# Kernel tuning notes

Hardware: AMD Instinct MI355X
Metric: run time of the kernel (lower is better)

The kernel has to match this reference:

```python
import jax, jax.numpy as jnp
import numpy as np

HIDDEN = 51
INPUT = 1
OUTPUT = 1
BATCH = 4096
SEQ = 999


def setup_inputs() -> dict:
    key = jax.random.key(0)
    ks = jax.random.split(key, 7)
    s = 1.0 / np.sqrt(HIDDEN)  # PyTorch default LSTM/Linear init scale
    u = lambda k, shape: jax.random.uniform(k, shape, jnp.float32, -s, s)
    return {
        "input": jax.random.normal(ks[0], (BATCH, SEQ, INPUT), jnp.float32),
        "W_ih": u(ks[1], (4 * HIDDEN, INPUT)),
        "W_hh": u(ks[2], (4 * HIDDEN, HIDDEN)),
        "b_ih": u(ks[3], (4 * HIDDEN,)),
        "b_hh": u(ks[4], (4 * HIDDEN,)),
        "W_fc": u(ks[5], (OUTPUT, HIDDEN)),
        "b_fc": u(ks[6], (OUTPUT,)),
        "future": 0,
    }


def reference(input, W_ih, W_hh, b_ih, b_hh, W_fc, b_fc, future):
    # Single-layer LSTM (PyTorch gate order i, f, g, o) scanned over time,
    # followed by a per-timestep Linear -> (batch, seq+future, output).
    def step(carry, x_t):
        h, c = carry
        gates = x_t @ W_ih.T + b_ih + h @ W_hh.T + b_hh  # (B, 4H)
        i, f, g, o = jnp.split(gates, 4, axis=-1)
        c = jax.nn.sigmoid(f) * c + jax.nn.sigmoid(i) * jnp.tanh(g)
        h = jax.nn.sigmoid(o) * jnp.tanh(c)
        return (h, c), h

    B = input.shape[0]
    h0 = jnp.zeros((B, HIDDEN), input.dtype)
    c0 = jnp.zeros((B, HIDDEN), input.dtype)
    xs = jnp.swapaxes(input, 0, 1)  # (T, B, I)
    (h, c), hs = jax.lax.scan(step, (h0, c0), xs)
    ys = hs @ W_fc.T + b_fc  # (T, B, O)

    # static Python int, so a trace-time loop is fine).
    y = ys[-1]
    extra = []
    for _ in range(future):
        (h, c), hn = step((h, c), y)
        y = hn @ W_fc.T + b_fc
        extra.append(y)
    if extra:
        ys = jnp.concatenate([ys, jnp.stack(extra, 0)], axis=0)
    return jnp.swapaxes(ys, 0, 1)  # (B, T+future, O)
```

## Files before the change

### kernel.cpp

```cpp
#include <hip/hip_runtime.h>
#include <hip/hip_bf16.h>

#define HID   51
#define MR    208
#define SEQT  999
#define CH    111
#define NCH   9
#define EPB   16
#define XST   17
#define NTH   448
#define BSTR  72

typedef __attribute__((ext_vector_type(8))) short  short8;
typedef __attribute__((ext_vector_type(4))) float  floatx4;
typedef __attribute__((ext_vector_type(2))) float  floatx2;

__global__ void prep_kernel(const float* __restrict__ W_hh,
                            const float* __restrict__ W_ih,
                            const float* __restrict__ W_fc,
                            __hip_bfloat16* __restrict__ A_ext)
{
    const float K1 = 1.442695040889f;
    int idx = blockIdx.x * blockDim.x + threadIdx.x;
    if (idx >= MR * 64) return;
    int r = idx >> 6, k = idx & 63;
    int T = r >> 4, r16 = r & 15, g4r = r16 >> 2, gate = r16 & 3;
    float v = 0.f;
    if (T < 12) {
        int u = ((T >> 1) << 3) + 2 * g4r + (T & 1);
        float s = (gate == 2) ? (-2.f * K1) : (-K1);
        if (k < HID)      v = s * W_hh[(gate * HID + u) * HID + k];
        else if (k == 51) v = s * W_ih[gate * HID + u];
    } else {
        if (g4r < 3) {
            int u = 48 + g4r;
            float s = (gate == 2) ? (-2.f * K1) : (-K1);
            if (k < HID)      v = s * W_hh[(gate * HID + u) * HID + k];
            else if (k == 51) v = s * W_ih[gate * HID + u];
        } else if (gate == 0) {
            if (k < HID) v = W_fc[k];
        }
    }
    A_ext[idx] = __float2bfloat16(v);
}

__launch_bounds__(NTH)
__global__ void lstm_mfma_kernel(const float* __restrict__ x,
                                 const float* __restrict__ b_ih,
                                 const float* __restrict__ b_hh,
                                 const float* __restrict__ b_fc,
                                 const __hip_bfloat16* __restrict__ A_ext,
                                 float* __restrict__ out)
{
    __shared__ __hip_bfloat16 bcol[2][16 * BSTR];
    __shared__ float x_lds[(CH + 1) * XST];
    __shared__ float y_lds[CH * XST];

    const int tid  = threadIdx.x;
    const int w    = tid >> 6;
    const int lane = tid & 63;
    const int e    = lane & 15;
    const int g4   = lane >> 4;
    const int e0   = blockIdx.x * EPB;
    const bool w6  = (w == 6);
    const int  uB6   = 48 + g4;
    const bool yln   = w6 && (g4 == 3);
    const bool xsv   = w6 && (g4 == 0);
    const int  wrow6 = (uB6 < HID) ? uB6 : 63;

    const float K1  = 1.442695040889f;
    const float K2N = -2.885390081777f;
    const floatx4 z4 = {0.f, 0.f, 0.f, 0.f};

    short8  A0a = {0,0,0,0,0,0,0,0}, A1a = {0,0,0,0,0,0,0,0};
    short8  A0b = {0,0,0,0,0,0,0,0}, A1b = {0,0,0,0,0,0,0,0};
    floatx4 bqa = {0.f, 0.f, 0.f, 0.f}, bqb = {0.f, 0.f, 0.f, 0.f};
    floatx2 cs2 = {0.f, 0.f};
    float   cs6 = 0.f;
    int ua = 0;

    if (!w6) {
        int Ta = 2 * w, Tb = 2 * w + 1;
        ua = 8 * w + 2 * g4;
        int ma = Ta * 16 + e, mb = Tb * 16 + e;
        A0a = *(const short8*)&A_ext[ma * 64 + g4 * 8];
        A1a = *(const short8*)&A_ext[ma * 64 + 32 + g4 * 8];
        A0b = *(const short8*)&A_ext[mb * 64 + g4 * 8];
        A1b = *(const short8*)&A_ext[mb * 64 + 32 + g4 * 8];
#pragma unroll
        for (int gg = 0; gg < 4; ++gg) {
            float s = (gg == 2) ? (-2.f * K1) : (-K1);
            bqa[gg] = s * (b_ih[gg * HID + ua]     + b_hh[gg * HID + ua]);
            bqb[gg] = s * (b_ih[gg * HID + ua + 1] + b_hh[gg * HID + ua + 1]);
        }
    } else {
        int m = 12 * 16 + e;
        A0a = *(const short8*)&A_ext[m * 64 + g4 * 8];
        A1a = *(const short8*)&A_ext[m * 64 + 32 + g4 * 8];
        if (uB6 < HID) {
#pragma unroll
            for (int gg = 0; gg < 4; ++gg) {
                float s = (gg == 2) ? (-2.f * K1) : (-K1);
                bqa[gg] = s * (b_ih[gg * HID + uB6] + b_hh[gg * HID + uB6]);
            }
        }
    }

    for (int i = tid; i < 16 * BSTR; i += NTH) {
        bcol[0][i] = __float2bfloat16(0.f);
        bcol[1][i] = __float2bfloat16(0.f);
    }
    __syncthreads();
    if (tid < EPB)
        bcol[0][tid * BSTR + 51] = __float2bfloat16(x[(size_t)(e0 + tid) * SEQT]);
    for (int i2 = tid; i2 < (CH + 1) * EPB; i2 += NTH) {
        int ee = i2 / (CH + 1), tt = i2 % (CH + 1);
        x_lds[tt * XST + ee] = x[(size_t)(e0 + ee) * SEQT + tt];
    }
    const float bfc = b_fc[0];

    __syncthreads();

    for (int tc = 0; tc < NCH; ++tc) {
        const int t0 = tc * CH;

        float xpre[4];
        {
            const int t0n = t0 + CH;
#pragma unroll
            for (int q = 0; q < 4; ++q) {
                int i2 = tid + q * NTH;
                int ee = i2 / (CH + 1), tt = i2 - ee * (CH + 1);
                int t = t0n + tt;
                xpre[q] = (t < SEQT) ? x[(size_t)(e0 + ee) * SEQT + t] : 0.f;
            }
        }

        for (int tt = 0; tt < CH; ++tt) {
            const int t  = t0 + tt;
            const int rp = t & 1, wp = rp ^ 1;

            short8 B0 = *(const short8*)&bcol[rp][e * BSTR + g4 * 8];
            short8 B1 = *(const short8*)&bcol[rp][e * BSTR + 32 + g4 * 8];

            if (!w6) {
                floatx4 aa = __builtin_amdgcn_mfma_f32_16x16x32_bf16(A0a, B0, bqa, 0, 0, 0);
                floatx4 a2 = __builtin_amdgcn_mfma_f32_16x16x32_bf16(A1a, B1, z4,  0, 0, 0);
                floatx4 ab = __builtin_amdgcn_mfma_f32_16x16x32_bf16(A0b, B0, bqb, 0, 0, 0);
                floatx4 b2 = __builtin_amdgcn_mfma_f32_16x16x32_bf16(A1b, B1, z4,  0, 0, 0);

                floatx4 sa = aa + a2;
                floatx4 sb = ab + b2;

                float EiA = __builtin_amdgcn_exp2f(sa[0]);
                float EiB = __builtin_amdgcn_exp2f(sb[0]);
                float EfA = __builtin_amdgcn_exp2f(sa[1]);
                float EfB = __builtin_amdgcn_exp2f(sb[1]);
                float EgA = __builtin_amdgcn_exp2f(sa[2]);
                float EgB = __builtin_amdgcn_exp2f(sb[2]);
                float EoA = __builtin_amdgcn_exp2f(sa[3]);
                float EoB = __builtin_amdgcn_exp2f(sb[3]);

                floatx2 Ei2 = {EiA, EiB};
                floatx2 Ef2 = {EfA, EfB};
                floatx2 Eg2 = {EgA, EgB};
                floatx2 Eo2 = {EoA, EoB};

                floatx2 t2  = (Ei2 + Eg2) + 1.f;
                floatx2 P2  = __builtin_elementwise_fma(Ei2, Eg2, t2);
                floatx2 F12 = Ef2 + 1.f;
                floatx2 D2  = F12 * P2;
                floatx2 R2  = {__builtin_amdgcn_rcpf(D2[0]),
                               __builtin_amdgcn_rcpf(D2[1])};
                floatx2 T2  = (1.f - Eg2) * F12;
                cs2 = __builtin_elementwise_fma(cs2, P2, K2N * T2) * R2;

                floatx2 Ec2 = {__builtin_amdgcn_exp2f(cs2[0]),
                               __builtin_amdgcn_exp2f(cs2[1])};
                floatx2 u2  = (Eo2 + Ec2) + 1.f;
                floatx2 D3  = __builtin_elementwise_fma(Eo2, Ec2, u2);
                floatx2 Ro2 = {__builtin_amdgcn_rcpf(D3[0]),
                               __builtin_amdgcn_rcpf(D3[1])};
                floatx2 h2  = (1.f - Ec2) * Ro2;

                unsigned hpk;
                asm("v_cvt_pk_bf16_f32 %0, %1, %2" : "=v"(hpk) : "v"(h2[0]), "v"(h2[1]));
                *(unsigned*)&bcol[wp][e * BSTR + ua] = hpk;
            } else {
                floatx4 acc = __builtin_amdgcn_mfma_f32_16x16x32_bf16(A0a, B0, bqa, 0, 0, 0);
                floatx4 ac2 = __builtin_amdgcn_mfma_f32_16x16x32_bf16(A1a, B1, z4,  0, 0, 0);

                float s0 = acc[0] + ac2[0];
                float Ei = __builtin_amdgcn_exp2f(s0);
                float Ef = __builtin_amdgcn_exp2f(acc[1] + ac2[1]);
                float Eg = __builtin_amdgcn_exp2f(acc[2] + ac2[2]);
                float Eo = __builtin_amdgcn_exp2f(acc[3] + ac2[3]);
                float P  = fmaf(Ei, Eg, (Ei + Eg) + 1.f);
                float F1 = 1.f + Ef;
                float R  = __builtin_amdgcn_rcpf(F1 * P);
                cs6 = fmaf(cs6, P, K2N * ((1.f - Eg) * F1)) * R;
                float Ec  = __builtin_amdgcn_exp2f(cs6);
                float Roc = __builtin_amdgcn_rcpf(fmaf(Eo, Ec, (Eo + Ec) + 1.f));
                float h   = (1.f - Ec) * Roc;

                bcol[wp][e * BSTR + wrow6] = __float2bfloat16((uB6 < HID) ? h : 0.f);
                if (yln) y_lds[tt * XST + e] = s0 + bfc;
                if (xsv) bcol[wp][e * BSTR + 51] =
                             __float2bfloat16(x_lds[(tt + 1) * XST + e]);
            }

            __syncthreads();
        }

        for (int i2 = tid; i2 < CH * EPB; i2 += NTH) {
            int ee = i2 / CH, tt = i2 % CH;
            int t = t0 + tt - 1;
            if (t >= 0)
                out[(size_t)(e0 + ee) * SEQT + t] = y_lds[tt * XST + ee];
        }
#pragma unroll
        for (int q = 0; q < 4; ++q) {
            int i2 = tid + q * NTH;
            int ee = i2 / (CH + 1), tt = i2 - ee * (CH + 1);
            x_lds[tt * XST + ee] = xpre[q];
        }
        __syncthreads();
    }

    if (w6) {
        short8 B0 = *(const short8*)&bcol[1][e * BSTR + g4 * 8];
        short8 B1 = *(const short8*)&bcol[1][e * BSTR + 32 + g4 * 8];
        floatx4 acc = __builtin_amdgcn_mfma_f32_16x16x32_bf16(A0a, B0, bqa, 0, 0, 0);
        acc = __builtin_amdgcn_mfma_f32_16x16x32_bf16(A1a, B1, acc, 0, 0, 0);
        if (g4 == 3)
            out[(size_t)(e0 + e) * SEQT + (SEQT - 1)] = acc[0] + bfc;
    }
}

extern "C" void kernel_launch(void* const* d_in, const int* in_sizes, int n_in,
                              void* d_out, int out_size, void* d_ws, size_t ws_size,
                              hipStream_t stream) {
    const float* x    = (const float*)d_in[0];
    const float* W_ih = (const float*)d_in[1];
    const float* W_hh = (const float*)d_in[2];
    const float* b_ih = (const float*)d_in[3];
    const float* b_hh = (const float*)d_in[4];
    const float* W_fc = (const float*)d_in[5];
    const float* b_fc = (const float*)d_in[6];
    float* out = (float*)d_out;

    __hip_bfloat16* A_ext = (__hip_bfloat16*)d_ws;

    prep_kernel<<<(MR * 64 + 255) / 256, 256, 0, stream>>>(W_hh, W_ih, W_fc, A_ext);
    lstm_mfma_kernel<<<4096 / EPB, NTH, 0, stream>>>(x, b_ih, b_hh,
                                                     b_fc, A_ext, out);
}
```

Baseline: 428.5 us.

## Stream x/y directly from global per step and drop chunked LDS staging

Removes the chunked x/y LDS staging buffers and the per-chunk bulk load/store phases. The x values are prefetched into registers three steps ahead, and each y is written straight to global memory from the lanes that compute it. The time loop is unrolled by two so the ping-pong buffer index is a compile-time constant. __syncthreads is replaced with an inline s_waitcnt lgkmcnt(0) plus s_barrier that does not wait on outstanding global stores. This removes the periodic serialized copy phases, but adds a scattered 4-byte global store and load on one wave every step.

```diff
diff --git a/kernel.cpp b/kernel.cpp
--- a/kernel.cpp
+++ b/kernel.cpp
@@ -4,10 +4,7 @@
 #define HID   51
 #define MR    208
 #define SEQT  999
-#define CH    111
-#define NCH   9
 #define EPB   16
-#define XST   17
 #define NTH   448
 #define BSTR  72
 
@@ -53,8 +50,6 @@
                                  float* __restrict__ out)
 {
     __shared__ __hip_bfloat16 bcol[2][16 * BSTR];
-    __shared__ float x_lds[(CH + 1) * XST];
-    __shared__ float y_lds[CH * XST];
 
     const int tid  = threadIdx.x;
     const int w    = tid >> 6;
@@ -63,10 +58,9 @@
     const int g4   = lane >> 4;
     const int e0   = blockIdx.x * EPB;
     const bool w6  = (w == 6);
-    const int  uB6   = 48 + g4;
-    const bool yln   = w6 && (g4 == 3);
-    const bool xsv   = w6 && (g4 == 0);
-    const int  wrow6 = (uB6 < HID) ? uB6 : 63;
+    const int  uB6 = 48 + g4;
+    const bool yln = w6 && (g4 == 3);
+    const bool xsv = w6 && (g4 == 0);
 
     const float K1  = 1.442695040889f;
     const float K2N = -2.885390081777f;
@@ -106,6 +100,13 @@
         }
     }
 
+    const float* xp = x   + (size_t)(e0 + e) * SEQT;
+    float*       yp = out + (size_t)(e0 + e) * SEQT;
+    const float  bfc = b_fc[0];
+
+    float xa = 0.f, xb = 0.f;
+    if (xsv) { xa = xp[1]; xb = xp[2]; }
+
     for (int i = tid; i < 16 * BSTR; i += NTH) {
         bcol[0][i] = __float2bfloat16(0.f);
         bcol[1][i] = __float2bfloat16(0.f);
@@ -113,119 +114,94 @@
     __syncthreads();
     if (tid < EPB)
         bcol[0][tid * BSTR + 51] = __float2bfloat16(x[(size_t)(e0 + tid) * SEQT]);
-    for (int i2 = tid; i2 < (CH + 1) * EPB; i2 += NTH) {
-        int ee = i2 / (CH + 1), tt = i2 % (CH + 1);
-        x_lds[tt * XST + ee] = x[(size_t)(e0 + ee) * SEQT + tt];
-    }
-    const float bfc = b_fc[0];
-
     __syncthreads();
 
-    for (int tc = 0; tc < NCH; ++tc) {
-        const int t0 = tc * CH;
-
-        float xpre[4];
-        {
-            const int t0n = t0 + CH;
-#pragma unroll
-            for (int q = 0; q < 4; ++q) {
-                int i2 = tid + q * NTH;
-                int ee = i2 / (CH + 1), tt = i2 - ee * (CH + 1);
-                int t = t0n + tt;
-                xpre[q] = (t < SEQT) ? x[(size_t)(e0 + ee) * SEQT + t] : 0.f;
+    auto STEP = [&](int t, int rp) {
+        const int wp = rp ^ 1;
+
+        short8 B0 = *(const short8*)&bcol[rp][e * BSTR + g4 * 8];
+        short8 B1 = *(const short8*)&bcol[rp][e * BSTR + 32 + g4 * 8];
+
+        if (!w6) {
+            floatx4 aa = __builtin_amdgcn_mfma_f32_16x16x32_bf16(A0a, B0, bqa, 0, 0, 0);
+            floatx4 a2 = __builtin_amdgcn_mfma_f32_16x16x32_bf16(A1a, B1, z4,  0, 0, 0);
+            floatx4 ab = __builtin_amdgcn_mfma_f32_16x16x32_bf16(A0b, B0, bqb, 0, 0, 0);
+            floatx4 b2 = __builtin_amdgcn_mfma_f32_16x16x32_bf16(A1b, B1, z4,  0, 0, 0);
+
+            floatx4 sa = aa + a2;
+            floatx4 sb = ab + b2;
+
+            float EiA = __builtin_amdgcn_exp2f(sa[0]);
+            float EiB = __builtin_amdgcn_exp2f(sb[0]);
+            float EfA = __builtin_amdgcn_exp2f(sa[1]);
+            float EfB = __builtin_amdgcn_exp2f(sb[1]);
+            float EgA = __builtin_amdgcn_exp2f(sa[2]);
+            float EgB = __builtin_amdgcn_exp2f(sb[2]);
+            float EoA = __builtin_amdgcn_exp2f(sa[3]);
+            float EoB = __builtin_amdgcn_exp2f(sb[3]);
+
+            floatx2 Ei2 = {EiA, EiB};
+            floatx2 Ef2 = {EfA, EfB};
+            floatx2 Eg2 = {EgA, EgB};
+            floatx2 Eo2 = {EoA, EoB};
+
+            floatx2 t2  = (Ei2 + Eg2) + 1.f;
+            floatx2 P2  = __builtin_elementwise_fma(Ei2, Eg2, t2);
+            floatx2 F12 = Ef2 + 1.f;
+            floatx2 D2  = F12 * P2;
+            floatx2 R2  = {__builtin_amdgcn_rcpf(D2[0]),
+                           __builtin_amdgcn_rcpf(D2[1])};
+            floatx2 T2  = (1.f - Eg2) * F12;
+            cs2 = __builtin_elementwise_fma(cs2, P2, K2N * T2) * R2;
+
+            floatx2 Ec2 = {__builtin_amdgcn_exp2f(cs2[0]),
+                           __builtin_amdgcn_exp2f(cs2[1])};
+            floatx2 u2  = (Eo2 + Ec2) + 1.f;
+            floatx2 D3  = __builtin_elementwise_fma(Eo2, Ec2, u2);
+            floatx2 Ro2 = {__builtin_amdgcn_rcpf(D3[0]),
+                           __builtin_amdgcn_rcpf(D3[1])};
+            floatx2 h2  = (1.f - Ec2) * Ro2;
+
+            unsigned hpk;
+            asm("v_cvt_pk_bf16_f32 %0, %1, %2" : "=v"(hpk) : "v"(h2[0]), "v"(h2[1]));
+            *(unsigned*)&bcol[wp][e * BSTR + ua] = hpk;
+        } else {
+            floatx4 acc = __builtin_amdgcn_mfma_f32_16x16x32_bf16(A0a, B0, bqa, 0, 0, 0);
+            floatx4 ac2 = __builtin_amdgcn_mfma_f32_16x16x32_bf16(A1a, B1, z4,  0, 0, 0);
+
+            float s0 = acc[0] + ac2[0];
+            float Ei = __builtin_amdgcn_exp2f(s0);
+            float Ef = __builtin_amdgcn_exp2f(acc[1] + ac2[1]);
+            float Eg = __builtin_amdgcn_exp2f(acc[2] + ac2[2]);
+            float Eo = __builtin_amdgcn_exp2f(acc[3] + ac2[3]);
+            float P  = fmaf(Ei, Eg, (Ei + Eg) + 1.f);
+            float F1 = 1.f + Ef;
+            float R  = __builtin_amdgcn_rcpf(F1 * P);
+            cs6 = fmaf(cs6, P, K2N * ((1.f - Eg) * F1)) * R;
+            float Ec  = __builtin_amdgcn_exp2f(cs6);
+            float Roc = __builtin_amdgcn_rcpf(fmaf(Eo, Ec, (Eo + Ec) + 1.f));
+            float h   = (1.f - Ec) * Roc;
+
+            if (uB6 < HID)
+                bcol[wp][e * BSTR + uB6] = __float2bfloat16(h);
+            if (yln && t > 0)
+                yp[t - 1] = s0 + bfc;
+            if (xsv) {
+                bcol[wp][e * BSTR + 51] = __float2bfloat16(xa);
+                xa = xb;
+                int tn = t + 3; tn = (tn > SEQT - 1) ? (SEQT - 1) : tn;
+                xb = xp[tn];
             }
         }
 
-        for (int tt = 0; tt < CH; ++tt) {
-            const int t  = t0 + tt;
-            const int rp = t & 1, wp = rp ^ 1;
-
-            short8 B0 = *(const short8*)&bcol[rp][e * BSTR + g4 * 8];
-            short8 B1 = *(const short8*)&bcol[rp][e * BSTR + 32 + g4 * 8];
-
-            if (!w6) {
-                floatx4 aa = __builtin_amdgcn_mfma_f32_16x16x32_bf16(A0a, B0, bqa, 0, 0, 0);
-                floatx4 a2 = __builtin_amdgcn_mfma_f32_16x16x32_bf16(A1a, B1, z4,  0, 0, 0);
-                floatx4 ab = __builtin_amdgcn_mfma_f32_16x16x32_bf16(A0b, B0, bqb, 0, 0, 0);
-                floatx4 b2 = __builtin_amdgcn_mfma_f32_16x16x32_bf16(A1b, B1, z4,  0, 0, 0);
-
-                floatx4 sa = aa + a2;
-                floatx4 sb = ab + b2;
-
-                float EiA = __builtin_amdgcn_exp2f(sa[0]);
-                float EiB = __builtin_amdgcn_exp2f(sb[0]);
-                float EfA = __builtin_amdgcn_exp2f(sa[1]);
-                float EfB = __builtin_amdgcn_exp2f(sb[1]);
-                float EgA = __builtin_amdgcn_exp2f(sa[2]);
-                float EgB = __builtin_amdgcn_exp2f(sb[2]);
-                float EoA = __builtin_amdgcn_exp2f(sa[3]);
-                float EoB = __builtin_amdgcn_exp2f(sb[3]);
-
-                floatx2 Ei2 = {EiA, EiB};
-                floatx2 Ef2 = {EfA, EfB};
-                floatx2 Eg2 = {EgA, EgB};
-                floatx2 Eo2 = {EoA, EoB};
-
-                floatx2 t2  = (Ei2 + Eg2) + 1.f;
-                floatx2 P2  = __builtin_elementwise_fma(Ei2, Eg2, t2);
-                floatx2 F12 = Ef2 + 1.f;
-                floatx2 D2  = F12 * P2;
-                floatx2 R2  = {__builtin_amdgcn_rcpf(D2[0]),
-                               __builtin_amdgcn_rcpf(D2[1])};
-                floatx2 T2  = (1.f - Eg2) * F12;
-                cs2 = __builtin_elementwise_fma(cs2, P2, K2N * T2) * R2;
-
-                floatx2 Ec2 = {__builtin_amdgcn_exp2f(cs2[0]),
-                               __builtin_amdgcn_exp2f(cs2[1])};
-                floatx2 u2  = (Eo2 + Ec2) + 1.f;
-                floatx2 D3  = __builtin_elementwise_fma(Eo2, Ec2, u2);
-                floatx2 Ro2 = {__builtin_amdgcn_rcpf(D3[0]),
-                               __builtin_amdgcn_rcpf(D3[1])};
-                floatx2 h2  = (1.f - Ec2) * Ro2;
-
-                unsigned hpk;
-                asm("v_cvt_pk_bf16_f32 %0, %1, %2" : "=v"(hpk) : "v"(h2[0]), "v"(h2[1]));
-                *(unsigned*)&bcol[wp][e * BSTR + ua] = hpk;
-            } else {
-                floatx4 acc = __builtin_amdgcn_mfma_f32_16x16x32_bf16(A0a, B0, bqa, 0, 0, 0);
-                floatx4 ac2 = __builtin_amdgcn_mfma_f32_16x16x32_bf16(A1a, B1, z4,  0, 0, 0);
-
-                float s0 = acc[0] + ac2[0];
-                float Ei = __builtin_amdgcn_exp2f(s0);
-                float Ef = __builtin_amdgcn_exp2f(acc[1] + ac2[1]);
-                float Eg = __builtin_amdgcn_exp2f(acc[2] + ac2[2]);
-                float Eo = __builtin_amdgcn_exp2f(acc[3] + ac2[3]);
-                float P  = fmaf(Ei, Eg, (Ei + Eg) + 1.f);
-                float F1 = 1.f + Ef;
-                float R  = __builtin_amdgcn_rcpf(F1 * P);
-                cs6 = fmaf(cs6, P, K2N * ((1.f - Eg) * F1)) * R;
-                float Ec  = __builtin_amdgcn_exp2f(cs6);
-                float Roc = __builtin_amdgcn_rcpf(fmaf(Eo, Ec, (Eo + Ec) + 1.f));
-                float h   = (1.f - Ec) * Roc;
-
-                bcol[wp][e * BSTR + wrow6] = __float2bfloat16((uB6 < HID) ? h : 0.f);
-                if (yln) y_lds[tt * XST + e] = s0 + bfc;
-                if (xsv) bcol[wp][e * BSTR + 51] =
-                             __float2bfloat16(x_lds[(tt + 1) * XST + e]);
-            }
-
-            __syncthreads();
-        }
-
-        for (int i2 = tid; i2 < CH * EPB; i2 += NTH) {
-            int ee = i2 / CH, tt = i2 % CH;
-            int t = t0 + tt - 1;
-            if (t >= 0)
-                out[(size_t)(e0 + ee) * SEQT + t] = y_lds[tt * XST + ee];
-        }
-#pragma unroll
-        for (int q = 0; q < 4; ++q) {
-            int i2 = tid + q * NTH;
-            int ee = i2 / (CH + 1), tt = i2 - ee * (CH + 1);
-            x_lds[tt * XST + ee] = xpre[q];
-        }
-        __syncthreads();
-    }
+        asm volatile("s_waitcnt lgkmcnt(0)\n\ts_barrier" ::: "memory");
+    };
+
+    for (int t = 0; t < SEQT - 1; t += 2) {
+        STEP(t, 0);
+        STEP(t + 1, 1);
+    }
+    STEP(SEQT - 1, 0);
 
     if (w6) {
         short8 B0 = *(const short8*)&bcol[1][e * BSTR + g4 * 8];
```

New measurement: 547.9 us. 27.9% more time.

## Rebalance gate tiles across eight waves and use lightweight step barrier

Applied to the files above, without the earlier changes.

Raises the block from 7 to 8 waves and redistributes the 13 gate tiles, so waves 4 and 6 take one tile each instead of two, shortening the critical path of the slowest wave per timestep. The x-prefetch loops gain bounds guards because 4*512 threads exceed the chunk size. The per-step __syncthreads is replaced with an inline s_waitcnt lgkmcnt(0) + s_barrier to cut barrier overhead. The extra wave adds barrier participants and register pressure, and the hand-written barrier relies on LDS ordering being covered only by lgkmcnt.

```diff
diff --git a/kernel.cpp b/kernel.cpp
--- a/kernel.cpp
+++ b/kernel.cpp
@@ -8,7 +8,7 @@
 #define NCH   9
 #define EPB   16
 #define XST   17
-#define NTH   448
+#define NTH   512
 #define BSTR  72
 
 typedef __attribute__((ext_vector_type(8))) short  short8;
@@ -62,11 +62,18 @@
     const int e    = lane & 15;
     const int g4   = lane >> 4;
     const int e0   = blockIdx.x * EPB;
-    const bool w6  = (w == 6);
-    const int  uB6   = 48 + g4;
-    const bool yln   = w6 && (g4 == 3);
-    const bool xsv   = w6 && (g4 == 0);
-    const int  wrow6 = (uB6 < HID) ? uB6 : 63;
+
+    const bool dual = (w < 4) || (w == 5);
+    const bool w7   = (w == 7);
+    int Ta, ur;
+    if      (w < 4)  { Ta = 2 * w; ur = 8 * w + 2 * g4; }
+    else if (w == 5) { Ta = 8;     ur = 32 + 2 * g4;    }
+    else if (w == 4) { Ta = 10;    ur = 40 + 2 * g4;    }
+    else if (w == 6) { Ta = 11;    ur = 41 + 2 * g4;    }
+    else             { Ta = 12;    ur = 48 + g4;        }
+    const bool yln   = w7 && (g4 == 3);
+    const bool xsv   = w7 && (g4 == 0);
+    const int  wrow7 = (ur < HID) ? ur : 63;
 
     const float K1  = 1.442695040889f;
     const float K2N = -2.885390081777f;
@@ -76,33 +83,25 @@
     short8  A0b = {0,0,0,0,0,0,0,0}, A1b = {0,0,0,0,0,0,0,0};
     floatx4 bqa = {0.f, 0.f, 0.f, 0.f}, bqb = {0.f, 0.f, 0.f, 0.f};
     floatx2 cs2 = {0.f, 0.f};
-    float   cs6 = 0.f;
-    int ua = 0;
-
-    if (!w6) {
-        int Ta = 2 * w, Tb = 2 * w + 1;
-        ua = 8 * w + 2 * g4;
-        int ma = Ta * 16 + e, mb = Tb * 16 + e;
+    float   cs1 = 0.f;
+
+    {
+        int ma = Ta * 16 + e;
         A0a = *(const short8*)&A_ext[ma * 64 + g4 * 8];
         A1a = *(const short8*)&A_ext[ma * 64 + 32 + g4 * 8];
-        A0b = *(const short8*)&A_ext[mb * 64 + g4 * 8];
-        A1b = *(const short8*)&A_ext[mb * 64 + 32 + g4 * 8];
+        if (dual) {
+            int mb = (Ta + 1) * 16 + e;
+            A0b = *(const short8*)&A_ext[mb * 64 + g4 * 8];
+            A1b = *(const short8*)&A_ext[mb * 64 + 32 + g4 * 8];
+        }
+    }
+    if (ur < HID) {
 #pragma unroll
         for (int gg = 0; gg < 4; ++gg) {
             float s = (gg == 2) ? (-2.f * K1) : (-K1);
-            bqa[gg] = s * (b_ih[gg * HID + ua]     + b_hh[gg * HID + ua]);
-            bqb[gg] = s * (b_ih[gg * HID + ua + 1] + b_hh[gg * HID + ua + 1]);
-        }
-    } else {
-        int m = 12 * 16 + e;
-        A0a = *(const short8*)&A_ext[m * 64 + g4 * 8];
-        A1a = *(const short8*)&A_ext[m * 64 + 32 + g4 * 8];
-        if (uB6 < HID) {
-#pragma unroll
-            for (int gg = 0; gg < 4; ++gg) {
-                float s = (gg == 2) ? (-2.f * K1) : (-K1);
-                bqa[gg] = s * (b_ih[gg * HID + uB6] + b_hh[gg * HID + uB6]);
-            }
+            bqa[gg] = s * (b_ih[gg * HID + ur] + b_hh[gg * HID + ur]);
+            if (dual)
+                bqb[gg] = s * (b_ih[gg * HID + ur + 1] + b_hh[gg * HID + ur + 1]);
         }
     }
 
@@ -130,9 +129,12 @@
 #pragma unroll
             for (int q = 0; q < 4; ++q) {
                 int i2 = tid + q * NTH;
-                int ee = i2 / (CH + 1), tt = i2 - ee * (CH + 1);
-                int t = t0n + tt;
-                xpre[q] = (t < SEQT) ? x[(size_t)(e0 + ee) * SEQT + t] : 0.f;
+                xpre[q] = 0.f;
+                if (i2 < (CH + 1) * EPB) {
+                    int ee = i2 / (CH + 1), tt = i2 - ee * (CH + 1);
+                    int t = t0n + tt;
+                    if (t < SEQT) xpre[q] = x[(size_t)(e0 + ee) * SEQT + t];
+                }
             }
         }
 
@@ -143,7 +145,7 @@
             short8 B0 = *(const short8*)&bcol[rp][e * BSTR + g4 * 8];
             short8 B1 = *(const short8*)&bcol[rp][e * BSTR + 32 + g4 * 8];
 
-            if (!w6) {
+            if (dual) {
                 floatx4 aa = __builtin_amdgcn_mfma_f32_16x16x32_bf16(A0a, B0, bqa, 0, 0, 0);
                 floatx4 a2 = __builtin_amdgcn_mfma_f32_16x16x32_bf16(A1a, B1, z4,  0, 0, 0);
                 floatx4 ab = __builtin_amdgcn_mfma_f32_16x16x32_bf16(A0b, B0, bqb, 0, 0, 0);
@@ -185,7 +187,7 @@
 
                 unsigned hpk;
                 asm("v_cvt_pk_bf16_f32 %0, %1, %2" : "=v"(hpk) : "v"(h2[0]), "v"(h2[1]));
-                *(unsigned*)&bcol[wp][e * BSTR + ua] = hpk;
+                *(unsigned*)&bcol[wp][e * BSTR + ur] = hpk;
             } else {
                 floatx4 acc = __builtin_amdgcn_mfma_f32_16x16x32_bf16(A0a, B0, bqa, 0, 0, 0);
                 floatx4 ac2 = __builtin_amdgcn_mfma_f32_16x16x32_bf16(A1a, B1, z4,  0, 0, 0);
@@ -198,18 +200,22 @@
                 float P  = fmaf(Ei, Eg, (Ei + Eg) + 1.f);
                 float F1 = 1.f + Ef;
                 float R  = __builtin_amdgcn_rcpf(F1 * P);
-                cs6 = fmaf(cs6, P, K2N * ((1.f - Eg) * F1)) * R;
-                float Ec  = __builtin_amdgcn_exp2f(cs6);
+                cs1 = fmaf(cs1, P, K2N * ((1.f - Eg) * F1)) * R;
+                float Ec  = __builtin_amdgcn_exp2f(cs1);
                 float Roc = __builtin_amdgcn_rcpf(fmaf(Eo, Ec, (Eo + Ec) + 1.f));
                 float h   = (1.f - Ec) * Roc;
 
-                bcol[wp][e * BSTR + wrow6] = __float2bfloat16((uB6 < HID) ? h : 0.f);
-                if (yln) y_lds[tt * XST + e] = s0 + bfc;
-                if (xsv) bcol[wp][e * BSTR + 51] =
-                             __float2bfloat16(x_lds[(tt + 1) * XST + e]);
+                if (!w7) {
+                    bcol[wp][e * BSTR + ur] = __float2bfloat16(h);
+                } else {
+                    bcol[wp][e * BSTR + wrow7] = __float2bfloat16((ur < HID) ? h : 0.f);
+                    if (yln) y_lds[tt * XST + e] = s0 + bfc;
+                    if (xsv) bcol[wp][e * BSTR + 51] =
+                                 __float2bfloat16(x_lds[(tt + 1) * XST + e]);
+                }
             }
 
-            __syncthreads();
+            asm volatile("s_waitcnt lgkmcnt(0)\n\ts_barrier" ::: "memory");
         }
 
         for (int i2 = tid; i2 < CH * EPB; i2 += NTH) {
@@ -221,13 +227,15 @@
 #pragma unroll
         for (int q = 0; q < 4; ++q) {
             int i2 = tid + q * NTH;
-            int ee = i2 / (CH + 1), tt = i2 - ee * (CH + 1);
-            x_lds[tt * XST + ee] = xpre[q];
+            if (i2 < (CH + 1) * EPB) {
+                int ee = i2 / (CH + 1), tt = i2 - ee * (CH + 1);
+                x_lds[tt * XST + ee] = xpre[q];
+            }
         }
         __syncthreads();
     }
 
-    if (w6) {
+    if (w7) {
         short8 B0 = *(const short8*)&bcol[1][e * BSTR + g4 * 8];
         short8 B1 = *(const short8*)&bcol[1][e * BSTR + 32 + g4 * 8];
         floatx4 acc = __builtin_amdgcn_mfma_f32_16x16x32_bf16(A0a, B0, bqa, 0, 0, 0);
```

New measurement: 450.4 us. 5.1% more time.
